# Kernel tuning notes

Hardware: AMD Instinct MI355X
Metric: run time of the kernel (lower is better)

## Reference

```python
import jax, jax.numpy as jnp
import numpy as np

CONF = 0.25      # args.conf
IOU_THR = 0.45   # args.iou
MAX_DET = 300    # args.max_det
NC = 80          # len(model.names)
CAND = 2048      # static cap: top-scoring candidates entering NMS (jit-friendly stand-in for boolean conf mask)


def setup_inputs():
    key = jax.random.key(0)
    pred = jax.random.uniform(key, (16, 4 + NC, 8400), dtype=jnp.float32)
    # first 4 channels are xywh in pixel coordinates for a 640x640 image
    pred = pred.at[:, :4, :].multiply(640.0)
    return {"pred": pred, "img_size": 640}


def xywh2xyxy(b):
    xy, wh = b[..., :2], b[..., 2:4]
    return jnp.concatenate([xy - wh * 0.5, xy + wh * 0.5], axis=-1)


def box_iou(b):
    # b: (K, 4) xyxy -> (K, K) pairwise IoU (torchvision convention)
    x1, y1, x2, y2 = b[:, 0], b[:, 1], b[:, 2], b[:, 3]
    area = (x2 - x1) * (y2 - y1)
    ix1 = jnp.maximum(x1[:, None], x1[None, :])
    iy1 = jnp.maximum(y1[:, None], y1[None, :])
    ix2 = jnp.minimum(x2[:, None], x2[None, :])
    iy2 = jnp.minimum(y2[:, None], y2[None, :])
    inter = jnp.clip(ix2 - ix1, 0.0) * jnp.clip(iy2 - iy1, 0.0)
    return inter / (area[:, None] + area[None, :] - inter + 1e-7)


def nms_keep(nmsbox, valid):
    # Greedy NMS over boxes already sorted by descending score.
    iou = box_iou(nmsbox)  # (CAND, CAND)

    def body(keep, i):
        suppressed = jnp.any(keep & (iou[i] > IOU_THR))
        ki = valid[i] & jnp.logical_not(suppressed)
        return keep.at[i].set(ki), None

    keep0 = jnp.zeros((nmsbox.shape[0],), dtype=bool)
    keep, _ = jax.lax.scan(body, keep0, jnp.arange(nmsbox.shape[0]))
    return keep


def _forward(pred, img_size):
    p = jnp.transpose(pred, (0, 2, 1))           # (N, A, 4+NC)
    boxes_xywh = p[..., :4]
    cls_scores = p[..., 4:4 + NC]
    scores = jnp.max(cls_scores, axis=-1)        # (N, A)
    classes = jnp.argmax(cls_scores, axis=-1)    # (N, A) int

    # static top-CAND candidates (score > conf handled via valid mask below)
    top_s, top_i = jax.lax.top_k(scores, CAND)   # sorted descending
    box = jnp.take_along_axis(boxes_xywh, top_i[..., None], axis=1)  # (N, CAND, 4)
    cls = jnp.take_along_axis(classes, top_i, axis=1)                # (N, CAND)
    box = xywh2xyxy(box)
    inv = 1.0 / img_size                          # multiplier=1, divide by max(H, W)

    def per_image(box_i, score_i, cls_i):
        valid = score_i > CONF
        # class-aware NMS: add class id offset to all 4 normalized coords
        nmsbox = box_i * inv + cls_i[:, None].astype(box_i.dtype)
        keep = nms_keep(nmsbox, valid)
        # kept boxes first, in score order; rest pushed to the end and zeroed
        order = jnp.argsort(jnp.where(keep, jnp.arange(CAND), CAND))[:MAX_DET]
        kept = keep[order].astype(box_i.dtype)[:, None]
        dets = jnp.concatenate(
            [box_i[order], score_i[order, None], cls_i[order, None].astype(box_i.dtype)],
            axis=-1,
        )  # (MAX_DET, 6)
        return dets * kept

    return jax.vmap(per_image)(box, top_s, cls)   # (N, MAX_DET, 6)


def reference(pred, img_size):
    return _forward(pred, img_size)
```

## Files before the change

### kernel.cpp

```cpp
#include <hip/hip_runtime.h>
#include <stdint.h>

#define NB 16
#define NA 8400
#define NA_PAD 9216
#define NCH 84
#define NCLS 80
#define CANDN 2048
#define MAXDET 300

typedef unsigned long long u64;

static const size_t OFF_SU   = 0;
static const size_t OFF_CLS  = 537600;
static const size_t OFF_BOX  = 1075200;
static const size_t OFF_KEY  = 3225600;
static const size_t OFF_NMSB = 3487744;
static const size_t OFF_AREA = 4012032;
static const size_t OFF_H12  = 4143104;
static const size_t OFF_H16  = 4405248;

__global__ __launch_bounds__(256) void score_kernel(const float* __restrict__ pred,
                                                    unsigned* __restrict__ sug,
                                                    int* __restrict__ cls,
                                                    float4* __restrict__ boxT,
                                                    int* __restrict__ h12,
                                                    int* __restrict__ h16) {
  int a = blockIdx.x * 256 + threadIdx.x;
  int b = blockIdx.y;
  if (a >= NA) return;
  int lane = threadIdx.x & 63;
  const float* pbase = pred + (size_t)b * (NCH * NA);
  const float* p = pbase + 4 * NA + a;
  float best = p[0];
  int bc = 0;
#pragma unroll 8
  for (int c = 1; c < NCLS; ++c) {
    float v = p[(size_t)c * NA];
    if (v > best) { best = v; bc = c; }
  }
  unsigned u = ~__float_as_uint(best);
  sug[(size_t)b * NA + a] = u;
  cls[(size_t)b * NA + a] = bc;
  boxT[(size_t)b * NA + a] =
      make_float4(pbase[a], pbase[NA + a], pbase[2 * NA + a], pbase[3 * NA + a]);
  u64 m = __ballot(true);
  u64 m12 = 0;
#pragma unroll
  for (int bit = 31; bit >= 16; --bit) {
    u64 bb = __ballot((u >> bit) & 1);
    m &= ((u >> bit) & 1) ? bb : ~bb;
    if (bit == 20) m12 = m;
  }
  u64 below = (lane == 0) ? 0ULL : ((1ULL << lane) - 1ULL);
  if ((m12 & below) == 0ULL)
    atomicAdd(&h12[b * 4096 + (int)(u >> 20)], (int)__popcll(m12));
  if ((m & below) == 0ULL)
    atomicAdd(&h16[b * 65536 + (int)(u >> 16)], (int)__popcll(m));
}

__device__ inline u64 shflx64(u64 v, int m) {
  int lo = __shfl_xor((int)(unsigned)(v & 0xFFFFFFFFu), m, 64);
  int hi = __shfl_xor((int)(unsigned)(v >> 32), m, 64);
  return (((u64)(unsigned)hi) << 32) | (unsigned)lo;
}

__device__ inline u64 cswap(u64 a, u64 b, int s, int j, int kk) {
  bool low = (s & j) == 0;
  bool asc = (s & kk) == 0;
  bool takeMin = (low == asc);
  u64 mn = (a < b) ? a : b;
  u64 mx = (a < b) ? b : a;
  return takeMin ? mn : mx;
}

__device__ inline bool iou_gt(float4 bi, float ai, float4 bj, float aj) {
  const double THR = 0x1.CCCCCC8p-2;
  float ix1 = fmaxf(bi.x, bj.x);
  float iy1 = fmaxf(bi.y, bj.y);
  float ix2 = fminf(bi.z, bj.z);
  float iy2 = fminf(bi.w, bj.w);
  float iw = fmaxf(__fsub_rn(ix2, ix1), 0.0f);
  float ih = fmaxf(__fsub_rn(iy2, iy1), 0.0f);
  float inter = __fmul_rn(iw, ih);
  float den = __fadd_rn(__fsub_rn(__fadd_rn(ai, aj), inter), 1e-7f);
  return (double)inter > THR * (double)den;
}

__global__ __launch_bounds__(1024) void select_kernel(const unsigned* __restrict__ sug,
                                                      const int* __restrict__ h12g,
                                                      const int* __restrict__ h16g,
                                                      u64* __restrict__ keybuf) {
  __shared__ alignas(16) unsigned su[NA];
  __shared__ int hist8[256];
  __shared__ int cum[256];
  __shared__ int tielist[1024];
  __shared__ int sl16[16];
  __shared__ int wtot[16];
  __shared__ unsigned sh_pref;
  __shared__ int sh_k, sh_g, sh_cnt;

  int b = blockIdx.x;
  int tid = threadIdx.x;
  int lane = tid & 63;
  int wv = tid >> 6;

  if (tid == 0) { sh_pref = 0; sh_k = CANDN; sh_g = 0; sh_cnt = 0; }

  {
    uint4* su4 = (uint4*)su;
    const uint4* sg4 = (const uint4*)(sug + (size_t)b * NA);
    for (int v = tid; v < NA / 4; v += 1024) su4[v] = sg4[v];
  }

  const int* hb = h12g + b * 4096;
  int4 v = ((const int4*)hb)[tid];
  int ssum = v.x + v.y + v.z + v.w;
  int incl = ssum;
  for (int off = 1; off < 64; off <<= 1) {
    int t = __shfl_up(incl, off, 64);
    if (lane >= off) incl += t;
  }
  if (lane == 63) wtot[wv] = incl;
  __syncthreads();
  if (tid < 16) {
    int w0 = wtot[tid];
    int inc2 = w0;
    for (int off = 1; off < 16; off <<= 1) {
      int t = __shfl_up(inc2, off, 16);
      if (tid >= off) inc2 += t;
    }
    wtot[tid] = inc2 - w0;
  }
  __syncthreads();
  int ebase = wtot[wv] + incl - ssum;
  if (ebase < CANDN && ebase + ssum >= CANDN) {
    int c = ebase;
    int hh[4] = {v.x, v.y, v.z, v.w};
#pragma unroll
    for (int t = 0; t < 4; ++t) {
      if (c + hh[t] >= CANDN) { sh_pref = (unsigned)(tid * 4 + t); sh_k = CANDN - c; break; }
      c += hh[t];
    }
  }
  __syncthreads();
  unsigned B12 = sh_pref;
  int k = sh_k;

  if (tid < 16) sl16[tid] = h16g[(size_t)b * 65536 + B12 * 16 + tid];
  __syncthreads();
  if (tid == 0) {
    int c = 0;
#pragma unroll
    for (int j = 0; j < 16; ++j) {
      int h = sl16[j];
      if (c + h >= k) { sh_pref = (B12 << 4) + (unsigned)j; sh_k = k - c; break; }
      c += h;
    }
  }
  __syncthreads();
  unsigned B16 = sh_pref;
  k = sh_k;

  if (tid < 256) hist8[tid] = 0;
  __syncthreads();
  for (int i = tid; i < NA; i += 1024) {
    unsigned u = su[i];
    if ((u >> 16) == B16) atomicAdd(&hist8[(u >> 8) & 255], 1);
  }
  __syncthreads();
  if (tid < 64) {
    int v0 = hist8[tid * 4 + 0], v1 = hist8[tid * 4 + 1];
    int v2 = hist8[tid * 4 + 2], v3 = hist8[tid * 4 + 3];
    int s0 = v0, s1 = s0 + v1, s2 = s1 + v2, s3 = s2 + v3;
    int tot = s3;
    for (int off = 1; off < 64; off <<= 1) {
      int t = __shfl_up(tot, off, 64);
      if (tid >= off) tot += t;
    }
    int base = tot - s3;
    cum[tid * 4 + 0] = base + s0;
    cum[tid * 4 + 1] = base + s1;
    cum[tid * 4 + 2] = base + s2;
    cum[tid * 4 + 3] = base + s3;
  }
  __syncthreads();
  if (tid < 256) {
    int c = cum[tid];
    int cprev = (tid == 0) ? 0 : cum[tid - 1];
    if (c >= k && cprev < k) {
      sh_pref = (B16 << 16) | ((unsigned)tid << 8);
      sh_k = k - cprev;
    }
  }
  __syncthreads();
  unsigned p24 = sh_pref;
  k = sh_k;

  if (tid < 256) hist8[tid] = 0;
  __syncthreads();
  for (int i = tid; i < NA; i += 1024) {
    unsigned u = su[i];
    if ((u & 0xFFFFFF00u) == p24) atomicAdd(&hist8[u & 255], 1);
  }
  __syncthreads();
  if (tid < 64) {
    int v0 = hist8[tid * 4 + 0], v1 = hist8[tid * 4 + 1];
    int v2 = hist8[tid * 4 + 2], v3 = hist8[tid * 4 + 3];
    int s0 = v0, s1 = s0 + v1, s2 = s1 + v2, s3 = s2 + v3;
    int tot = s3;
    for (int off = 1; off < 64; off <<= 1) {
      int t = __shfl_up(tot, off, 64);
      if (tid >= off) tot += t;
    }
    int base = tot - s3;
    cum[tid * 4 + 0] = base + s0;
    cum[tid * 4 + 1] = base + s1;
    cum[tid * 4 + 2] = base + s2;
    cum[tid * 4 + 3] = base + s3;
  }
  __syncthreads();
  if (tid < 256) {
    int c = cum[tid];
    int cprev = (tid == 0) ? 0 : cum[tid - 1];
    if (c >= k && cprev < k) {
      sh_pref = p24 | (unsigned)tid;
      sh_k = k - cprev;
    }
  }
  __syncthreads();
  unsigned ustar = sh_pref;
  int kp = sh_k;

  for (int i = tid; i < NA; i += 1024) {
    if (su[i] == ustar) {
      int p = atomicAdd(&sh_g, 1);
      if (p < 1024) tielist[p] = i;
    }
  }
  __syncthreads();
  int g = sh_g < 1024 ? sh_g : 1024;

  for (int i = tid; i < NA_PAD; i += 1024) {
    bool act = false;
    u64 key = 0;
    if (i < NA) {
      unsigned u = su[i];
      if (u < ustar) act = true;
      else if (u == ustar) {
        int r = 0;
        for (int t2 = 0; t2 < g; ++t2) r += (tielist[t2] < i);
        act = (r < kp);
      }
      key = (((u64)u) << 32) | (unsigned)i;
    }
    u64 mm = __ballot(act);
    if (mm) {
      int leader = __ffsll(mm) - 1;
      int base = 0;
      if (lane == leader) base = atomicAdd(&sh_cnt, (int)__popcll(mm));
      base = __shfl(base, leader, 64);
      if (act)
        keybuf[(size_t)b * CANDN + base + (int)__popcll(mm & ((1ULL << lane) - 1))] = key;
    }
  }
}

__global__ __launch_bounds__(256) void prep_kernel(const u64* __restrict__ keybuf,
                                                   const int* __restrict__ clsg,
                                                   const float4* __restrict__ boxTg,
                                                   const int* __restrict__ imgsz,
                                                   float4* __restrict__ nmsbG,
                                                   float* __restrict__ areaG) {
  int s = blockIdx.x * 256 + threadIdx.x;
  int b = blockIdx.y;
  int o = b * CANDN + s;
  u64 key = keybuf[o];
  int idx = (int)(unsigned)(key & 0xFFFFFFFFu);
  float4 bx = boxTg[(size_t)b * NA + idx];
  float inv = (float)(1.0 / (double)imgsz[0]);
  float hw = __fmul_rn(bx.z, 0.5f);
  float hh = __fmul_rn(bx.w, 0.5f);
  float x1 = __fsub_rn(bx.x, hw);
  float y1 = __fsub_rn(bx.y, hh);
  float x2 = __fadd_rn(bx.x, hw);
  float y2 = __fadd_rn(bx.y, hh);
  float clsf = (float)clsg[(size_t)b * NA + idx];
  float nx1 = __fadd_rn(__fmul_rn(x1, inv), clsf);
  float ny1 = __fadd_rn(__fmul_rn(y1, inv), clsf);
  float nx2 = __fadd_rn(__fmul_rn(x2, inv), clsf);
  float ny2 = __fadd_rn(__fmul_rn(y2, inv), clsf);
  float ar = __fmul_rn(__fsub_rn(nx2, nx1), __fsub_rn(ny2, ny1));
  nmsbG[o] = make_float4(nx1, ny1, nx2, ny2);
  areaG[o] = ar;
}

__global__ __launch_bounds__(1024) void nms_kernel(const u64* __restrict__ keybuf,
                                                   const float4* __restrict__ nmsbG,
                                                   const float* __restrict__ areaG,
                                                   const int* __restrict__ clsg,
                                                   const float4* __restrict__ boxTg,
                                                   float* __restrict__ out) {
  __shared__ alignas(16) u64 skey[CANDN];
  __shared__ alignas(16) float4 nmsb[CANDN];
  __shared__ float areaA[CANDN];
  __shared__ unsigned short a2s[NA];
  __shared__ float4 chunkbox[64];
  __shared__ float chunkarea[64];
  __shared__ float4 keptbox[MAXDET];
  __shared__ float keptarea[MAXDET];
  __shared__ int idxbuf[MAXDET];
  __shared__ u64 diag[64];
  __shared__ u64 supm[16];
  __shared__ int sh_nms;

  int b = blockIdx.x;
  int tid = threadIdx.x;
  int lane = tid & 63;
  int wv = tid >> 6;

  if (tid == 0) sh_nms = 0;

  for (int s = tid; s < CANDN; s += 1024) {
    u64 key = keybuf[(size_t)b * CANDN + s];
    skey[s] = key;
    nmsb[s] = nmsbG[(size_t)b * CANDN + s];
    areaA[s] = areaG[(size_t)b * CANDN + s];
    a2s[(unsigned)(key & 0xFFFFFFFFu)] = (unsigned short)s;
  }
  __syncthreads();

  int s0 = (wv << 7) + lane;
  int s1 = s0 + 64;
  u64 e0 = skey[s0];
  u64 e1 = skey[s1];
  for (int kk = 2; kk <= CANDN; kk <<= 1) {
    for (int j = kk >> 1; j > 0; j >>= 1) {
      if (j >= 128) {
        skey[s0] = e0;
        skey[s1] = e1;
        __syncthreads();
        u64 p0 = skey[s0 ^ j];
        u64 p1 = skey[s1 ^ j];
        e0 = cswap(e0, p0, s0, j, kk);
        e1 = cswap(e1, p1, s1, j, kk);
        __syncthreads();
      } else if (j == 64) {
        bool asc = (s0 & kk) == 0;
        u64 mn = (e0 < e1) ? e0 : e1;
        u64 mx = (e0 < e1) ? e1 : e0;
        e0 = asc ? mn : mx;
        e1 = asc ? mx : mn;
      } else {
        u64 p0 = shflx64(e0, j);
        u64 p1 = shflx64(e1, j);
        e0 = cswap(e0, p0, s0, j, kk);
        e1 = cswap(e1, p1, s1, j, kk);
      }
    }
  }
  skey[s0] = e0;
  skey[s1] = e1;
  __syncthreads();

#pragma unroll 1
  for (int c = 0; c < 32; ++c) {
    __syncthreads();
    int nk0 = sh_nms;
    if (nk0 >= MAXDET) break;
    int rank = (c << 6) + lane;
    u64 mykey = skey[rank];
    int slot = a2s[(unsigned)(mykey & 0xFFFFFFFFu)];
    float4 br = nmsb[slot];
    float arr = areaA[slot];
    if (wv == 0) { chunkbox[lane] = br; chunkarea[lane] = arr; }
    bool myvalid = __uint_as_float(~(unsigned)(mykey >> 32)) > 0.25f;
    bool sup = false;
    for (int q = wv; q < nk0; q += 16)
      sup = sup || iou_gt(br, arr, keptbox[q], keptarea[q]);
    u64 sm = __ballot(sup);
    if (lane == 0) supm[wv] = sm;
    __syncthreads();
#pragma unroll
    for (int rr = 0; rr < 4; ++rr) {
      int r = (wv << 2) + rr;
      bool supd = iou_gt(chunkbox[r], chunkarea[r], br, arr);
      u64 bb = __ballot(supd);
      if (lane == 0) diag[r] = bb;
    }
    u64 vb = __ballot(myvalid);
    __syncthreads();
    if (wv == 0) {
      u64 orsup = 0ULL;
#pragma unroll
      for (int w = 0; w < 16; ++w) orsup |= supm[w];
      bool tent = (((vb >> lane) & 1ULL) != 0ULL) &&
                  (((orsup >> lane) & 1ULL) == 0ULL);
      u64 below = (lane == 0) ? 0ULL : ((1ULL << lane) - 1ULL);
      u64 colbelow = diag[lane] & below;
      u64 kept = __ballot(tent);
      for (int it = 0; it < 64; ++it) {
        bool alive = tent && ((kept & colbelow) == 0ULL);
        u64 nk = __ballot(alive);
        if (nk == kept) break;
        kept = nk;
      }
      int nadd = (int)__popcll(kept);
      int cnt = nk0 + nadd;
      if (cnt > MAXDET) cnt = MAXDET;
      bool mine = ((kept >> lane) & 1ULL) != 0ULL;
      int pos = nk0 + (int)__popcll(kept & below);
      if (mine && pos < MAXDET) {
        idxbuf[pos] = rank;
        keptbox[pos] = br;
        keptarea[pos] = arr;
      }
      if (lane == 0) sh_nms = cnt;
    }
  }
  __syncthreads();

  int total = sh_nms;
  if (tid < MAXDET) {
    float vals[6] = {0.f, 0.f, 0.f, 0.f, 0.f, 0.f};
    if (tid < total) {
      int rank = idxbuf[tid];
      u64 key = skey[rank];
      int idx = (int)(unsigned)(key & 0xFFFFFFFFu);
      float score = __uint_as_float(~(unsigned)(key >> 32));
      float4 bx = boxTg[(size_t)b * NA + idx];
      float hw = __fmul_rn(bx.z, 0.5f);
      float hh = __fmul_rn(bx.w, 0.5f);
      vals[0] = __fsub_rn(bx.x, hw);
      vals[1] = __fsub_rn(bx.y, hh);
      vals[2] = __fadd_rn(bx.x, hw);
      vals[3] = __fadd_rn(bx.y, hh);
      vals[4] = score;
      vals[5] = (float)clsg[(size_t)b * NA + idx];
    }
#pragma unroll
    for (int q = 0; q < 6; ++q)
      out[((size_t)(b * MAXDET) + tid) * 6 + q] = vals[q];
  }
}

extern "C" void kernel_launch(void* const* d_in, const int* in_sizes, int n_in,
                              void* d_out, int out_size, void* d_ws, size_t ws_size,
                              hipStream_t stream) {
  (void)in_sizes; (void)n_in; (void)out_size; (void)ws_size;
  const float* pred = (const float*)d_in[0];
  const int* imgsz = (const int*)d_in[1];
  char* ws = (char*)d_ws;
  unsigned* sug = (unsigned*)(ws + OFF_SU);
  int* cls = (int*)(ws + OFF_CLS);
  float4* boxT = (float4*)(ws + OFF_BOX);
  u64* keybuf = (u64*)(ws + OFF_KEY);
  float4* nmsbG = (float4*)(ws + OFF_NMSB);
  float* areaG = (float*)(ws + OFF_AREA);
  int* h12 = (int*)(ws + OFF_H12);
  int* h16 = (int*)(ws + OFF_H16);
  float* out = (float*)d_out;

  hipMemsetAsync(h12, 0, (size_t)(262144 + 4194304), stream);
  score_kernel<<<dim3((NA + 255) / 256, NB), 256, 0, stream>>>(pred, sug, cls, boxT,
                                                               h12, h16);
  select_kernel<<<NB, 1024, 0, stream>>>(sug, h12, h16, keybuf);
  prep_kernel<<<dim3(CANDN / 256, NB), 256, 0, stream>>>(keybuf, cls, boxT, imgsz,
                                                         nmsbG, areaG);
  nms_kernel<<<NB, 1024, 0, stream>>>(keybuf, nmsbG, areaG, cls, boxT, out);
}
```

Before: 69.65 us.

## Drop global 16-bit histogram; refine radix select with 8-bit and 12-bit passes in LDS

Removes the 65536-bin per-image global histogram, so the 4.4 MB memset and its atomics go away; a small zero kernel now clears only the 12-bit histogram. The radix select in select_kernel now refines the threshold in two shared-memory passes: an 8-bit pass (bits 12-19, with ballot-aggregated atomics) and a 12-bit pass over the low bits. This trades global memory traffic and a large memset for extra LDS passes, and a 4096-entry LDS histogram plus scan inside the single-block-per-image select kernel.

Result: slower. 72.62 us (+4.3%).

```diff
diff --git a/kernel.cpp b/kernel.cpp
--- a/kernel.cpp
+++ b/kernel.cpp
@@ -18,14 +18,16 @@
 static const size_t OFF_NMSB = 3487744;
 static const size_t OFF_AREA = 4012032;
 static const size_t OFF_H12  = 4143104;
-static const size_t OFF_H16  = 4405248;
+
+__global__ __launch_bounds__(256) void zero_kernel(int* __restrict__ h12) {
+  h12[blockIdx.x * 256 + threadIdx.x] = 0;
+}
 
 __global__ __launch_bounds__(256) void score_kernel(const float* __restrict__ pred,
                                                     unsigned* __restrict__ sug,
                                                     int* __restrict__ cls,
                                                     float4* __restrict__ boxT,
-                                                    int* __restrict__ h12,
-                                                    int* __restrict__ h16) {
+                                                    int* __restrict__ h12) {
   int a = blockIdx.x * 256 + threadIdx.x;
   int b = blockIdx.y;
   if (a >= NA) return;
@@ -45,18 +47,14 @@
   boxT[(size_t)b * NA + a] =
       make_float4(pbase[a], pbase[NA + a], pbase[2 * NA + a], pbase[3 * NA + a]);
   u64 m = __ballot(true);
-  u64 m12 = 0;
-#pragma unroll
-  for (int bit = 31; bit >= 16; --bit) {
+#pragma unroll
+  for (int bit = 31; bit >= 20; --bit) {
     u64 bb = __ballot((u >> bit) & 1);
     m &= ((u >> bit) & 1) ? bb : ~bb;
-    if (bit == 20) m12 = m;
   }
   u64 below = (lane == 0) ? 0ULL : ((1ULL << lane) - 1ULL);
-  if ((m12 & below) == 0ULL)
-    atomicAdd(&h12[b * 4096 + (int)(u >> 20)], (int)__popcll(m12));
   if ((m & below) == 0ULL)
-    atomicAdd(&h16[b * 65536 + (int)(u >> 16)], (int)__popcll(m));
+    atomicAdd(&h12[b * 4096 + (int)(u >> 20)], (int)__popcll(m));
 }
 
 __device__ inline u64 shflx64(u64 v, int m) {
@@ -89,13 +87,11 @@
 
 __global__ __launch_bounds__(1024) void select_kernel(const unsigned* __restrict__ sug,
                                                       const int* __restrict__ h12g,
-                                                      const int* __restrict__ h16g,
                                                       u64* __restrict__ keybuf) {
   __shared__ alignas(16) unsigned su[NA];
-  __shared__ int hist8[256];
+  __shared__ int histL[4096];
   __shared__ int cum[256];
   __shared__ int tielist[1024];
-  __shared__ int sl16[16];
   __shared__ int wtot[16];
   __shared__ unsigned sh_pref;
   __shared__ int sh_k, sh_g, sh_cnt;
@@ -114,64 +110,66 @@
   }
 
   const int* hb = h12g + b * 4096;
-  int4 v = ((const int4*)hb)[tid];
-  int ssum = v.x + v.y + v.z + v.w;
-  int incl = ssum;
-  for (int off = 1; off < 64; off <<= 1) {
-    int t = __shfl_up(incl, off, 64);
-    if (lane >= off) incl += t;
-  }
-  if (lane == 63) wtot[wv] = incl;
-  __syncthreads();
-  if (tid < 16) {
-    int w0 = wtot[tid];
-    int inc2 = w0;
-    for (int off = 1; off < 16; off <<= 1) {
-      int t = __shfl_up(inc2, off, 16);
-      if (tid >= off) inc2 += t;
-    }
-    wtot[tid] = inc2 - w0;
-  }
-  __syncthreads();
-  int ebase = wtot[wv] + incl - ssum;
-  if (ebase < CANDN && ebase + ssum >= CANDN) {
-    int c = ebase;
-    int hh[4] = {v.x, v.y, v.z, v.w};
-#pragma unroll
-    for (int t = 0; t < 4; ++t) {
-      if (c + hh[t] >= CANDN) { sh_pref = (unsigned)(tid * 4 + t); sh_k = CANDN - c; break; }
-      c += hh[t];
+  {
+    int4 v = ((const int4*)hb)[tid];
+    int ssum = v.x + v.y + v.z + v.w;
+    int incl = ssum;
+    for (int off = 1; off < 64; off <<= 1) {
+      int t = __shfl_up(incl, off, 64);
+      if (lane >= off) incl += t;
+    }
+    if (lane == 63) wtot[wv] = incl;
+    __syncthreads();
+    if (tid < 16) {
+      int w0 = wtot[tid];
+      int inc2 = w0;
+      for (int off = 1; off < 16; off <<= 1) {
+        int t = __shfl_up(inc2, off, 16);
+        if (tid >= off) inc2 += t;
+      }
+      wtot[tid] = inc2 - w0;
+    }
+    __syncthreads();
+    int ebase = wtot[wv] + incl - ssum;
+    if (ebase < CANDN && ebase + ssum >= CANDN) {
+      int c = ebase;
+      int hh[4] = {v.x, v.y, v.z, v.w};
+#pragma unroll
+      for (int t = 0; t < 4; ++t) {
+        if (c + hh[t] >= CANDN) { sh_pref = (unsigned)(tid * 4 + t); sh_k = CANDN - c; break; }
+        c += hh[t];
+      }
     }
   }
   __syncthreads();
   unsigned B12 = sh_pref;
   int k = sh_k;
 
-  if (tid < 16) sl16[tid] = h16g[(size_t)b * 65536 + B12 * 16 + tid];
-  __syncthreads();
-  if (tid == 0) {
-    int c = 0;
-#pragma unroll
-    for (int j = 0; j < 16; ++j) {
-      int h = sl16[j];
-      if (c + h >= k) { sh_pref = (B12 << 4) + (unsigned)j; sh_k = k - c; break; }
-      c += h;
-    }
-  }
-  __syncthreads();
-  unsigned B16 = sh_pref;
-  k = sh_k;
-
-  if (tid < 256) hist8[tid] = 0;
-  __syncthreads();
-  for (int i = tid; i < NA; i += 1024) {
-    unsigned u = su[i];
-    if ((u >> 16) == B16) atomicAdd(&hist8[(u >> 8) & 255], 1);
+  if (tid < 256) histL[tid] = 0;
+  __syncthreads();
+  for (int i = tid; i < NA_PAD; i += 1024) {
+    bool act = false;
+    int d = 0;
+    if (i < NA) {
+      unsigned u = su[i];
+      act = (u >> 20) == B12;
+      d = (int)((u >> 12) & 255);
+    }
+    u64 m = __ballot(act);
+    if (m) {
+#pragma unroll
+      for (int bit = 0; bit < 8; ++bit) {
+        u64 bb = __ballot((d >> bit) & 1);
+        m &= ((d >> bit) & 1) ? bb : ~bb;
+      }
+      if (act && (m & ((1ULL << lane) - 1)) == 0ULL)
+        atomicAdd(&histL[d], (int)__popcll(m));
+    }
   }
   __syncthreads();
   if (tid < 64) {
-    int v0 = hist8[tid * 4 + 0], v1 = hist8[tid * 4 + 1];
-    int v2 = hist8[tid * 4 + 2], v3 = hist8[tid * 4 + 3];
+    int v0 = histL[tid * 4 + 0], v1 = histL[tid * 4 + 1];
+    int v2 = histL[tid * 4 + 2], v3 = histL[tid * 4 + 3];
     int s0 = v0, s1 = s0 + v1, s2 = s1 + v2, s3 = s2 + v3;
     int tot = s3;
     for (int off = 1; off < 64; off <<= 1) {
@@ -189,43 +187,56 @@
     int c = cum[tid];
     int cprev = (tid == 0) ? 0 : cum[tid - 1];
     if (c >= k && cprev < k) {
-      sh_pref = (B16 << 16) | ((unsigned)tid << 8);
+      sh_pref = (B12 << 8) | (unsigned)tid;
       sh_k = k - cprev;
     }
   }
   __syncthreads();
-  unsigned p24 = sh_pref;
+  unsigned B20 = sh_pref;
   k = sh_k;
 
-  if (tid < 256) hist8[tid] = 0;
+  for (int i = tid; i < 4096; i += 1024) histL[i] = 0;
   __syncthreads();
   for (int i = tid; i < NA; i += 1024) {
     unsigned u = su[i];
-    if ((u & 0xFFFFFF00u) == p24) atomicAdd(&hist8[u & 255], 1);
-  }
-  __syncthreads();
-  if (tid < 64) {
-    int v0 = hist8[tid * 4 + 0], v1 = hist8[tid * 4 + 1];
-    int v2 = hist8[tid * 4 + 2], v3 = hist8[tid * 4 + 3];
-    int s0 = v0, s1 = s0 + v1, s2 = s1 + v2, s3 = s2 + v3;
-    int tot = s3;
+    if ((u >> 12) == B20) atomicAdd(&histL[u & 4095], 1);
+  }
+  __syncthreads();
+  {
+    int bbase = tid * 4;
+    int h0 = histL[bbase + 0], h1 = histL[bbase + 1];
+    int h2 = histL[bbase + 2], h3 = histL[bbase + 3];
+    int ssum = h0 + h1 + h2 + h3;
+    int incl = ssum;
     for (int off = 1; off < 64; off <<= 1) {
-      int t = __shfl_up(tot, off, 64);
-      if (tid >= off) tot += t;
-    }
-    int base = tot - s3;
-    cum[tid * 4 + 0] = base + s0;
-    cum[tid * 4 + 1] = base + s1;
-    cum[tid * 4 + 2] = base + s2;
-    cum[tid * 4 + 3] = base + s3;
-  }
-  __syncthreads();
-  if (tid < 256) {
-    int c = cum[tid];
-    int cprev = (tid == 0) ? 0 : cum[tid - 1];
-    if (c >= k && cprev < k) {
-      sh_pref = p24 | (unsigned)tid;
-      sh_k = k - cprev;
+      int t = __shfl_up(incl, off, 64);
+      if (lane >= off) incl += t;
+    }
+    if (lane == 63) wtot[wv] = incl;
+    __syncthreads();
+    if (tid < 16) {
+      int w0 = wtot[tid];
+      int inc2 = w0;
+      for (int off = 1; off < 16; off <<= 1) {
+        int t = __shfl_up(inc2, off, 16);
+        if (tid >= off) inc2 += t;
+      }
+      wtot[tid] = inc2 - w0;
+    }
+    __syncthreads();
+    int ebase = wtot[wv] + incl - ssum;
+    if (ebase < k && ebase + ssum >= k) {
+      int c = ebase;
+      int hh[4] = {h0, h1, h2, h3};
+#pragma unroll
+      for (int t = 0; t < 4; ++t) {
+        if (c + hh[t] >= k) {
+          sh_pref = (B20 << 12) | (unsigned)(bbase + t);
+          sh_k = k - c;
+          break;
+        }
+        c += hh[t];
+      }
     }
   }
   __syncthreads();
@@ -458,13 +469,12 @@
   float4* nmsbG = (float4*)(ws + OFF_NMSB);
   float* areaG = (float*)(ws + OFF_AREA);
   int* h12 = (int*)(ws + OFF_H12);
-  int* h16 = (int*)(ws + OFF_H16);
   float* out = (float*)d_out;
 
-  hipMemsetAsync(h12, 0, (size_t)(262144 + 4194304), stream);
+  zero_kernel<<<256, 256, 0, stream>>>(h12);
   score_kernel<<<dim3((NA + 255) / 256, NB), 256, 0, stream>>>(pred, sug, cls, boxT,
-                                                               h12, h16);
-  select_kernel<<<NB, 1024, 0, stream>>>(sug, h12, h16, keybuf);
+                                                               h12);
+  select_kernel<<<NB, 1024, 0, stream>>>(sug, h12, keybuf);
   prep_kernel<<<dim3(CANDN / 256, NB), 256, 0, stream>>>(keybuf, cls, boxT, imgsz,
                                                          nmsbG, areaG);
   nms_kernel<<<NB, 1024, 0, stream>>>(keybuf, nmsbG, areaG, cls, boxT, out);
```

## Bucket kept boxes by class so NMS only checks neighbouring classes

Applied to the files above, without the earlier changes.

Kept boxes are stored in per-class shared-memory buckets of 16, with an overflow list, and each candidate is tested only against kept boxes in its own class and the two adjacent classes plus the overflow. This relies on the class offset making IoU zero across distant classes. It replaces the scan over all kept boxes spread across 16 waves. Diagonal IoU ballots are skipped for rows that are already suppressed, and the hipMemsetAsync is replaced by a custom zero kernel. In exchange, only four waves do the kept-box check, which may serialize when many boxes share one class, and it adds atomics and a byte class buffer.

Result: faster. 66.81 us (-4.1%).

```diff
diff --git a/kernel.cpp b/kernel.cpp
--- a/kernel.cpp
+++ b/kernel.cpp
@@ -19,6 +19,11 @@
 static const size_t OFF_AREA = 4012032;
 static const size_t OFF_H12  = 4143104;
 static const size_t OFF_H16  = 4405248;
+static const size_t OFF_CLSB = 8599552;
+
+__global__ __launch_bounds__(256) void zero_kernel(int* __restrict__ h) {
+  h[blockIdx.x * 256 + threadIdx.x] = 0;
+}
 
 __global__ __launch_bounds__(256) void score_kernel(const float* __restrict__ pred,
                                                     unsigned* __restrict__ sug,
@@ -271,7 +276,8 @@
                                                    const float4* __restrict__ boxTg,
                                                    const int* __restrict__ imgsz,
                                                    float4* __restrict__ nmsbG,
-                                                   float* __restrict__ areaG) {
+                                                   float* __restrict__ areaG,
+                                                   unsigned char* __restrict__ clsbG) {
   int s = blockIdx.x * 256 + threadIdx.x;
   int b = blockIdx.y;
   int o = b * CANDN + s;
@@ -285,7 +291,8 @@
   float y1 = __fsub_rn(bx.y, hh);
   float x2 = __fadd_rn(bx.x, hw);
   float y2 = __fadd_rn(bx.y, hh);
-  float clsf = (float)clsg[(size_t)b * NA + idx];
+  int ci = clsg[(size_t)b * NA + idx];
+  float clsf = (float)ci;
   float nx1 = __fadd_rn(__fmul_rn(x1, inv), clsf);
   float ny1 = __fadd_rn(__fmul_rn(y1, inv), clsf);
   float nx2 = __fadd_rn(__fmul_rn(x2, inv), clsf);
@@ -293,11 +300,13 @@
   float ar = __fmul_rn(__fsub_rn(nx2, nx1), __fsub_rn(ny2, ny1));
   nmsbG[o] = make_float4(nx1, ny1, nx2, ny2);
   areaG[o] = ar;
+  clsbG[o] = (unsigned char)ci;
 }
 
 __global__ __launch_bounds__(1024) void nms_kernel(const u64* __restrict__ keybuf,
                                                    const float4* __restrict__ nmsbG,
                                                    const float* __restrict__ areaG,
+                                                   const unsigned char* __restrict__ clsbG,
                                                    const int* __restrict__ clsg,
                                                    const float4* __restrict__ boxTg,
                                                    float* __restrict__ out) {
@@ -305,27 +314,34 @@
   __shared__ alignas(16) float4 nmsb[CANDN];
   __shared__ float areaA[CANDN];
   __shared__ unsigned short a2s[NA];
+  __shared__ unsigned char clsA[CANDN];
   __shared__ float4 chunkbox[64];
   __shared__ float chunkarea[64];
-  __shared__ float4 keptbox[MAXDET];
-  __shared__ float keptarea[MAXDET];
+  __shared__ float4 bbox[NCLS][16];
+  __shared__ float barea[NCLS][16];
+  __shared__ int bcount[NCLS];
+  __shared__ float4 ovfbox[MAXDET];
+  __shared__ float ovfarea[MAXDET];
   __shared__ int idxbuf[MAXDET];
   __shared__ u64 diag[64];
-  __shared__ u64 supm[16];
-  __shared__ int sh_nms;
+  __shared__ u64 supx[4];
+  __shared__ u64 vmaskc;
+  __shared__ int sh_nms, sh_ovf;
 
   int b = blockIdx.x;
   int tid = threadIdx.x;
   int lane = tid & 63;
   int wv = tid >> 6;
 
-  if (tid == 0) sh_nms = 0;
+  if (tid == 0) { sh_nms = 0; sh_ovf = 0; }
+  if (tid < NCLS) bcount[tid] = 0;
 
   for (int s = tid; s < CANDN; s += 1024) {
     u64 key = keybuf[(size_t)b * CANDN + s];
     skey[s] = key;
     nmsb[s] = nmsbG[(size_t)b * CANDN + s];
     areaA[s] = areaG[(size_t)b * CANDN + s];
+    clsA[s] = clsbG[(size_t)b * CANDN + s];
     a2s[(unsigned)(key & 0xFFFFFFFFu)] = (unsigned short)s;
   }
   __syncthreads();
@@ -373,29 +389,46 @@
     int slot = a2s[(unsigned)(mykey & 0xFFFFFFFFu)];
     float4 br = nmsb[slot];
     float arr = areaA[slot];
-    if (wv == 0) { chunkbox[lane] = br; chunkarea[lane] = arr; }
-    bool myvalid = __uint_as_float(~(unsigned)(mykey >> 32)) > 0.25f;
-    bool sup = false;
-    for (int q = wv; q < nk0; q += 16)
-      sup = sup || iou_gt(br, arr, keptbox[q], keptarea[q]);
-    u64 sm = __ballot(sup);
-    if (lane == 0) supm[wv] = sm;
+    int myc = clsA[slot];
+    if (wv == 0) {
+      chunkbox[lane] = br;
+      chunkarea[lane] = arr;
+      u64 vb = __ballot(__uint_as_float(~(unsigned)(mykey >> 32)) > 0.25f);
+      if (lane == 0) vmaskc = vb;
+    }
+    if (wv < 3) {
+      int cc = myc - 1 + wv;
+      bool ok = (cc >= 0 && cc < NCLS);
+      int n = ok ? bcount[cc] : 0;
+      bool sup = false;
+      for (int q = 0; q < n; ++q)
+        sup = sup || iou_gt(br, arr, bbox[cc][q], barea[cc][q]);
+      u64 sm = __ballot(sup);
+      if (lane == 0) supx[wv] = sm;
+    } else if (wv == 3) {
+      int n = sh_ovf;
+      bool sup = false;
+      for (int q = 0; q < n; ++q)
+        sup = sup || iou_gt(br, arr, ovfbox[q], ovfarea[q]);
+      u64 sm = __ballot(sup);
+      if (lane == 0) supx[3] = sm;
+    }
     __syncthreads();
+    u64 tentg = vmaskc & ~(supx[0] | supx[1] | supx[2] | supx[3]);
 #pragma unroll
     for (int rr = 0; rr < 4; ++rr) {
       int r = (wv << 2) + rr;
-      bool supd = iou_gt(chunkbox[r], chunkarea[r], br, arr);
-      u64 bb = __ballot(supd);
-      if (lane == 0) diag[r] = bb;
-    }
-    u64 vb = __ballot(myvalid);
+      if ((tentg >> r) & 1ULL) {
+        bool supd = iou_gt(chunkbox[r], chunkarea[r], br, arr);
+        u64 bb = __ballot(supd);
+        if (lane == 0) diag[r] = bb;
+      } else if (lane == 0) {
+        diag[r] = 0ULL;
+      }
+    }
     __syncthreads();
     if (wv == 0) {
-      u64 orsup = 0ULL;
-#pragma unroll
-      for (int w = 0; w < 16; ++w) orsup |= supm[w];
-      bool tent = (((vb >> lane) & 1ULL) != 0ULL) &&
-                  (((orsup >> lane) & 1ULL) == 0ULL);
+      bool tent = ((tentg >> lane) & 1ULL) != 0ULL;
       u64 below = (lane == 0) ? 0ULL : ((1ULL << lane) - 1ULL);
       u64 colbelow = diag[lane] & below;
       u64 kept = __ballot(tent);
@@ -405,15 +438,19 @@
         if (nk == kept) break;
         kept = nk;
       }
-      int nadd = (int)__popcll(kept);
-      int cnt = nk0 + nadd;
+      int cnt = nk0 + (int)__popcll(kept);
       if (cnt > MAXDET) cnt = MAXDET;
       bool mine = ((kept >> lane) & 1ULL) != 0ULL;
       int pos = nk0 + (int)__popcll(kept & below);
       if (mine && pos < MAXDET) {
         idxbuf[pos] = rank;
-        keptbox[pos] = br;
-        keptarea[pos] = arr;
+        int n = atomicAdd(&bcount[myc], 1);
+        if (n < 16) { bbox[myc][n] = br; barea[myc][n] = arr; }
+        else {
+          int mo = atomicAdd(&sh_ovf, 1);
+          ovfbox[mo] = br;
+          ovfarea[mo] = arr;
+        }
       }
       if (lane == 0) sh_nms = cnt;
     }
@@ -459,13 +496,14 @@
   float* areaG = (float*)(ws + OFF_AREA);
   int* h12 = (int*)(ws + OFF_H12);
   int* h16 = (int*)(ws + OFF_H16);
+  unsigned char* clsb = (unsigned char*)(ws + OFF_CLSB);
   float* out = (float*)d_out;
 
-  hipMemsetAsync(h12, 0, (size_t)(262144 + 4194304), stream);
+  zero_kernel<<<(262144 + 4194304) / 4 / 256, 256, 0, stream>>>(h12);
   score_kernel<<<dim3((NA + 255) / 256, NB), 256, 0, stream>>>(pred, sug, cls, boxT,
                                                                h12, h16);
   select_kernel<<<NB, 1024, 0, stream>>>(sug, h12, h16, keybuf);
   prep_kernel<<<dim3(CANDN / 256, NB), 256, 0, stream>>>(keybuf, cls, boxT, imgsz,
-                                                         nmsbG, areaG);
-  nms_kernel<<<NB, 1024, 0, stream>>>(keybuf, nmsbG, areaG, cls, boxT, out);
-}
+                                                         nmsbG, areaG, clsb);
+  nms_kernel<<<NB, 1024, 0, stream>>>(keybuf, nmsbG, areaG, clsb, cls, boxT, out);
+}
```
